# Optimization experiments

Measured on AMD Instinct MI355X. Metric: run time of the kernel, lower is better.

## Reference

```python
import jax, jax.numpy as jnp
import numpy as np

B, S, D, H, K = 1, 4096, 1024, 16, 64


def setup_inputs() -> dict:
    key = jax.random.key(0)
    ks = jax.random.split(key, 5)
    x = jax.random.normal(ks[0], (B, S, D), dtype=jnp.float32)
    wq = jax.random.normal(ks[1], (D, H, K), dtype=jnp.float32) / np.sqrt(D)
    wk = jax.random.normal(ks[2], (D, H, K), dtype=jnp.float32) / np.sqrt(D)
    wv = jax.random.normal(ks[3], (D, H, K), dtype=jnp.float32) / np.sqrt(D)
    wo = jax.random.normal(ks[4], (H, K, D), dtype=jnp.float32) / np.sqrt(H * K)
    bq = jnp.zeros((H, K), dtype=jnp.float32)
    bk = jnp.zeros((H, K), dtype=jnp.float32)
    bv = jnp.zeros((H, K), dtype=jnp.float32)
    bo = jnp.zeros((D,), dtype=jnp.float32)
    return {"x": x, "wq": wq, "bq": bq, "wk": wk, "bk": bk,
            "wv": wv, "bv": bv, "wo": wo, "bo": bo, "is_causal": 1}


def reference(x, wq, bq, wk, bk, wv, bv, wo, bo, is_causal):
    # QKV projections: [B,S,D] x [D,H,K] -> [B,S,H,K]
    q = jnp.einsum("bsd,dhk->bshk", x, wq) + bq
    k = jnp.einsum("bsd,dhk->bshk", x, wk) + bk
    v = jnp.einsum("bsd,dhk->bshk", x, wv) + bv
    # scores: [B,H,Q,KV], scaled by 1/sqrt(head_dim)
    scores = jnp.einsum("bqhk,bvhk->bhqv", q, k) / jnp.sqrt(jnp.float32(K))
    if is_causal:
        qpos = jnp.arange(S)[:, None]  # query position
        kpos = jnp.arange(S)[None, :]  # key position
        mask = (qpos >= kpos).astype(scores.dtype)  # [Q,KV]
        scores = scores - 1e9 * (1.0 - mask)
    probs = jax.nn.softmax(scores, axis=-1)
    # weighted values: [B,S,H,K]
    vals = jnp.einsum("bhqv,bvhk->bqhk", probs, v)
    # output projection: [B,S,H,K] x [H,K,D] -> [B,S,D]
    out = jnp.einsum("bqhk,hkd->bqd", vals, wo) + bo
    return out
```

## Files before the change

### kernel.cpp

```cpp
#include <hip/hip_runtime.h>

typedef _Float16 f16;
typedef f16 f16x8 __attribute__((ext_vector_type(8)));
typedef f16 f16x4 __attribute__((ext_vector_type(4)));
typedef float f32x2 __attribute__((ext_vector_type(2)));
typedef float f32x4 __attribute__((ext_vector_type(4)));
typedef float f32x16 __attribute__((ext_vector_type(16)));
typedef unsigned u32;

#define MFMA16(a, b, c) __builtin_amdgcn_mfma_f32_16x16x32_f16((a), (b), (c), 0, 0, 0)
#define MFMA32(a, b, c) __builtin_amdgcn_mfma_f32_32x32x16_f16((a), (b), (c), 0, 0, 0)

#define QSCL 0.18033688011f

#define WAITV(N) asm volatile("s_waitcnt vmcnt(" #N ")" ::: "memory")
#define BAR()                          \
  {                                    \
    __builtin_amdgcn_s_barrier();      \
    __builtin_amdgcn_sched_barrier(0); \
  }

__device__ __forceinline__ void gll16(const void* g, void* l) {
  __builtin_amdgcn_global_load_lds(
      (__attribute__((address_space(1))) unsigned int*)(void*)(g),
      (__attribute__((address_space(3))) unsigned int*)(l), 16, 0, 0);
}

__device__ __forceinline__ float ex2(float x) {
  float r;
  asm("v_exp_f32 %0, %1" : "=v"(r) : "v"(x));
  return r;
}

__device__ __forceinline__ void plswap(u32& a, u32& b) {
  asm("s_nop 1\n\tv_permlane32_swap_b32 %0, %1\n\ts_nop 1" : "+v"(a), "+v"(b));
}

__device__ __forceinline__ void plswap2(u32& a, u32& b, u32& c, u32& d) {
  asm("s_nop 1\n\tv_permlane32_swap_b32 %0, %1\n\tv_permlane32_swap_b32 %2, %3\n\ts_nop 1"
      : "+v"(a), "+v"(b), "+v"(c), "+v"(d));
}

__device__ __forceinline__ u32 pk16(float lo, float hi) {
  __fp16 h2[2];
  *(decltype(__builtin_amdgcn_cvt_pkrtz(0.f, 0.f))*)h2 =
      __builtin_amdgcn_cvt_pkrtz(lo, hi);
  return *(u32*)h2;
}

__global__ void k_prep(const float* __restrict__ x, f16* __restrict__ xb,
                       const float* __restrict__ wq, const float* __restrict__ wk,
                       const float* __restrict__ wv, const float* __restrict__ wo,
                       f16* __restrict__ wqkvT, f16* __restrict__ woT) {
  __shared__ float tile[64][65];
  const int bid = blockIdx.x;
  if (bid < 4096) {
    const int i = bid * 256 + threadIdx.x;
    float4 v = reinterpret_cast<const float4*>(x)[i];
    f16x4 o = {(f16)v.x, (f16)v.y, (f16)v.z, (f16)v.w};
    reinterpret_cast<f16x4*>(xb)[i] = o;
    return;
  }
  const int tb = bid - 4096;
  const int which = tb >> 8;
  const int bidx = tb & 255;
  const float* src = which == 0 ? wq : which == 1 ? wk : which == 2 ? wv : wo;
  f16* dst = which == 0 ? wqkvT
             : which == 1 ? wqkvT + (size_t)1024 * 1024
             : which == 2 ? wqkvT + (size_t)2048 * 1024
                          : woT;
  const int bc = bidx & 15, br = bidx >> 4;
  const int r0 = br << 6, c0 = bc << 6;
  const int tr = threadIdx.x >> 6, tc = threadIdx.x & 63;
#pragma unroll
  for (int p = 0; p < 16; ++p)
    tile[p * 4 + tr][tc] = src[(size_t)(r0 + p * 4 + tr) * 1024 + c0 + tc];
  __syncthreads();
#pragma unroll
  for (int p = 0; p < 16; ++p)
    dst[(size_t)(c0 + p * 4 + tr) * 1024 + r0 + tc] = (f16)tile[tc][p * 4 + tr];
}

template <int MODE, int NFR, int PAIR>
__global__ __launch_bounds__(256, 3) void k_gemm(
    const f16* __restrict__ A, const f16* __restrict__ Bt, int nbm, int Kd,
    const float* __restrict__ bias0, const float* __restrict__ bias1,
    const float* __restrict__ bias2,
    f16* __restrict__ Qo, f16* __restrict__ Ko, f16* __restrict__ Vo,
    float* __restrict__ Fo) {
  constexpr int TSZ = 8192 + NFR * 2048;
  constexpr int NBUF = PAIR ? 4 : 3;
  __shared__ __align__(16) char smem[NBUF * TSZ];
  const int tid = threadIdx.x;
  const int wid = tid >> 6, lane = tid & 63;
  const int r = lane & 15, t = lane >> 4;
  const int bm = blockIdx.x % nbm, bn = blockIdx.x / nbm;
  const int m0 = bm << 7, n0 = bn * (NFR * 32);
  const int wr = wid >> 1, wc = wid & 1;

  const f32x4 vz = {0.f, 0.f, 0.f, 0.f};
  f32x4 acc[4][NFR];
#pragma unroll
  for (int m = 0; m < 4; ++m)
#pragma unroll
    for (int n = 0; n < NFR; ++n) acc[m][n] = vz;

  const int srow = tid >> 2;
  const int scb = (((tid & 3) ^ ((tid >> 3) & 3)) << 4);
  const size_t ldb = (size_t)Kd * 2;
  const char* Ab = (const char*)A + (size_t)m0 * ldb + scb;
  const char* Bb = (const char*)Bt + (size_t)n0 * ldb + scb;

  auto issue = [&](int kt, int buf) {
    const size_t kb = (size_t)kt << 6;
    char* base = smem + buf * TSZ;
    gll16(Ab + (size_t)srow * ldb + kb, base + wid * 1024);
    gll16(Ab + (size_t)(srow + 64) * ldb + kb, base + 4096 + wid * 1024);
    gll16(Bb + (size_t)srow * ldb + kb, base + 8192 + wid * 1024);
    if (NFR == 4)
      gll16(Bb + (size_t)(srow + 64) * ldb + kb, base + 8192 + 4096 + wid * 1024);
  };

  const int swz = ((r >> 1) & 3) << 4;

  auto comp = [&](int buf) {
    const char* base = smem + buf * TSZ;
    f16x8 af[4], bg[NFR];
#pragma unroll
    for (int m = 0; m < 4; ++m)
      af[m] = *(const f16x8*)(base + ((wr * 64 + m * 16 + r) * 64 +
                                      ((t * 16) ^ swz)));
#pragma unroll
    for (int n = 0; n < NFR; ++n)
      bg[n] = *(const f16x8*)(base + 8192 +
                              ((wc * (NFR * 16) + n * 16 + r) * 64 +
                               ((t * 16) ^ swz)));
    __builtin_amdgcn_s_setprio(1);
#pragma unroll
    for (int m = 0; m < 4; ++m)
#pragma unroll
      for (int n = 0; n < NFR; ++n) acc[m][n] = MFMA16(af[m], bg[n], acc[m][n]);
    __builtin_amdgcn_s_setprio(0);
  };

  const int nk = Kd >> 5;
  if (PAIR) {
    issue(0, 0);
    issue(1, 1);
    const int nsup = nk >> 1;
    for (int T = 0; T < nsup; ++T) {
      WAITV(0);
      BAR();
      if (T + 1 < nsup) {
        issue(2 * T + 2, (2 * T + 2) & 3);
        issue(2 * T + 3, (2 * T + 3) & 3);
      }
      comp((2 * T) & 3);
      comp((2 * T + 1) & 3);
    }
  } else {
    issue(0, 0);
    issue(1, 1);
    int b = 0, bi = 2;
    for (int kt = 0; kt < nk; ++kt) {
      if (kt + 1 < nk) {
        if (NFR == 4) {
          WAITV(4);
        } else {
          WAITV(3);
        }
      } else {
        WAITV(0);
      }
      BAR();
      if (kt + 2 < nk) issue(kt + 2, bi);
      comp(b);
      b = (b == 2) ? 0 : b + 1;
      bi = (bi == 2) ? 0 : bi + 1;
    }
  }

#pragma unroll
  for (int m = 0; m < 4; ++m) {
    const int row0 = m0 + wr * 64 + m * 16 + t * 4;
#pragma unroll
    for (int n = 0; n < NFR; ++n) {
      const int gc = n0 + wc * (NFR * 16) + n * 16 + r;
      if (MODE == 0) {
        const float b2 = gc < 1024 ? bias0[gc]
                                   : (gc < 2048 ? bias1[gc - 1024] : bias2[gc - 2048]);
        float v[4];
#pragma unroll
        for (int i = 0; i < 4; ++i) v[i] = acc[m][n][i] + b2;
        if (gc < 1024) {
#pragma unroll
          for (int i = 0; i < 4; ++i)
            Qo[(size_t)(row0 + i) * 1024 + gc] = (f16)(v[i] * QSCL);
        } else if (gc < 2048) {
#pragma unroll
          for (int i = 0; i < 4; ++i)
            Ko[(size_t)(row0 + i) * 1024 + (gc - 1024)] = (f16)v[i];
        } else {
          f16x4 pk = {(f16)v[0], (f16)v[1], (f16)v[2], (f16)v[3]};
          *(f16x4*)(Vo + (size_t)(gc - 2048) * 4096 + row0) = pk;
        }
      } else {
        const float b2 = bias0[gc];
#pragma unroll
        for (int i = 0; i < 4; ++i)
          Fo[(size_t)(row0 + i) * 1024 + gc] = acc[m][n][i] + b2;
      }
    }
  }
}

__global__ __launch_bounds__(512, 4) void k_fattn(
    const f16* __restrict__ Q, const f16* __restrict__ Kb,
    const f16* __restrict__ Vt, f16* __restrict__ vals,
    const int* __restrict__ causp) {
  __shared__ uint4 ldsv[4128];
  char* lds = (char*)ldsv;
  const int tid = threadIdx.x;
  const int W = tid >> 6, lane = tid & 63;
  const int l31 = lane & 31, hi = lane >> 5;
  const int wq = W >> 1, wkv = W & 1;
  const int h = blockIdx.x & 15;
  const int idx = blockIdx.x >> 4;
  const int qt = idx < 16 ? 31 - idx : idx - 16;
  const int cz = *causp;
  const int Tmax = cz ? qt : 31;
  const int dw = wq - wkv;
  const int jmax_w = cz ? (2 * qt + (dw >= 2 ? 1 : 0) - (dw < 0 ? 1 : 0)) : 63;
  const bool maskd = cz && ((dw & 1) == 0);

  const size_t qrow = (size_t)((qt << 7) + (wq << 5) + l31) * 1024 + h * 64;
  f16x8 qf[4];
#pragma unroll
  for (int s = 0; s < 4; ++s) qf[s] = *(const f16x8*)(Q + qrow + 16 * s + 8 * hi);

  f32x16 o0, o1, zv;
#pragma unroll
  for (int e = 0; e < 16; ++e) { o0[e] = 0.f; o1[e] = 0.f; zv[e] = 0.f; }
  float Ls = 0.f;

  const int srw = lane >> 3, sch = lane & 7;
  const int ssw = (sch ^ srw) << 3;
  const char* kcur =
      (const char*)(Kb + (size_t)(8 * W + srw) * 1024 + h * 64 + ssw);
  const char* vcur =
      (const char*)(Vt + (size_t)(h * 64 + 8 * W + srw) * 4096 + ssw);

  auto issue = [&](int buf) {
    char* base = lds + buf * 16384 + W * 1024;
    gll16(kcur, base);
    gll16(vcur, base + 8192);
    kcur += (size_t)64 * 2048;
    vcur += 128;
  };

  const int krow = (wkv << 5) + l31, ksw = krow & 7;
  const int vsw = l31 & 7;
  int koff[4];
#pragma unroll
  for (int s = 0; s < 4; ++s)
    koff[s] = krow * 128 + (((2 * s + hi) ^ ksw) << 4);
  int voffA[2], voffB[2];
#pragma unroll
  for (int ks = 0; ks < 2; ++ks) {
    const int cl = 4 * wkv + 2 * ks + hi;
    voffA[ks] = l31 * 128 + ((cl ^ vsw) << 4);
    voffB[ks] = (32 + l31) * 128 + ((cl ^ vsw) << 4);
  }

  auto qk = [&](const char* Kbase) -> f32x16 {
    f16x8 af[4];
#pragma unroll
    for (int s = 0; s < 4; ++s)
      af[s] = *(const f16x8*)(Kbase + koff[s]);
    __builtin_amdgcn_s_setprio(1);
    f32x16 sc = MFMA32(af[0], qf[0], zv);
#pragma unroll
    for (int s = 1; s < 4; ++s) sc = MFMA32(af[s], qf[s], sc);
    __builtin_amdgcn_s_setprio(0);
    return sc;
  };

  auto fin = [&](int j, const char* Kbase, f32x16& sc) {
    const char* Vbase = Kbase + 8192;
    if (maskd && j == jmax_w) {
#pragma unroll
      for (int e = 0; e < 16; ++e) {
        const int kvr = (e & 3) + 8 * (e >> 2) + 4 * hi;
        if (kvr > l31) sc[e] = -1e9f;
      }
    }
    f32x2 p2[8];
#pragma unroll
    for (int e = 0; e < 8; ++e) {
      f32x2 t;
      t[0] = ex2(sc[2 * e]);
      t[1] = ex2(sc[2 * e + 1]);
      p2[e] = t;
    }
    {
      f32x2 a0 = p2[0] + p2[1];
      f32x2 a1 = p2[2] + p2[3];
      f32x2 a2 = p2[4] + p2[5];
      f32x2 a3 = p2[6] + p2[7];
      f32x2 b0 = a0 + a1;
      f32x2 b1 = a2 + a3;
      f32x2 c = b0 + b1;
      float s = c[0] + c[1];
      union { float f; u32 u; } ua, ub;
      ua.f = s; ub.f = s;
      plswap(ua.u, ub.u);
      Ls += ua.f + ub.f;
    }
#pragma unroll
    for (int ks = 0; ks < 2; ++ks) {
      u32 c0 = pk16(p2[4 * ks + 0][0], p2[4 * ks + 0][1]);
      u32 c1 = pk16(p2[4 * ks + 1][0], p2[4 * ks + 1][1]);
      u32 c2 = pk16(p2[4 * ks + 2][0], p2[4 * ks + 2][1]);
      u32 c3 = pk16(p2[4 * ks + 3][0], p2[4 * ks + 3][1]);
      plswap2(c0, c2, c1, c3);
      union { u32 w[4]; f16x8 v; } pa;
      pa.w[0] = c0; pa.w[1] = c1; pa.w[2] = c2; pa.w[3] = c3;
      const f16x8 vf0 = *(const f16x8*)(Vbase + voffA[ks]);
      const f16x8 vf1 = *(const f16x8*)(Vbase + voffB[ks]);
      __builtin_amdgcn_s_setprio(1);
      o0 = MFMA32(pa.v, vf0, o0);
      o1 = MFMA32(pa.v, vf1, o1);
      __builtin_amdgcn_s_setprio(0);
    }
  };

  issue(0);
  issue(1);

  for (int T = 0; T <= Tmax; ++T) {
    BAR();
    if (T < Tmax) {
      const int nb = 2 * ((T + 1) & 1);
      issue(nb);
      issue(nb + 1);
      WAITV(4);
    } else {
      WAITV(0);
    }
    const int cb = 2 * (T & 1);
    const char* bA = lds + cb * 16384;
    const char* bB = lds + (cb + 1) * 16384;
    const int jA = 2 * T, jB = 2 * T + 1;
    if (jB <= jmax_w) {
      f32x16 scA = qk(bA);
      f32x16 scB = qk(bB);
      fin(jA, bA, scA);
      fin(jB, bB, scB);
    } else if (jA <= jmax_w) {
      f32x16 scA = qk(bA);
      fin(jA, bA, scA);
    }
  }
  __syncthreads();

  float* obuf = (float*)lds;
  float* lsbuf = (float*)(lds + 32768);
  if (hi == 0) lsbuf[wq * 64 + wkv * 32 + l31] = Ls;
  if (wkv == 1) {
    float* base = obuf + wq * 2048;
#pragma unroll
    for (int dblk = 0; dblk < 2; ++dblk)
#pragma unroll
      for (int rg = 0; rg < 4; ++rg) {
        const f32x16& o = dblk ? o1 : o0;
        f32x4 t = {o[rg * 4 + 0], o[rg * 4 + 1], o[rg * 4 + 2], o[rg * 4 + 3]};
        *(f32x4*)(base + ((dblk * 4 + rg) * 64 + lane) * 4) = t;
      }
  }
  __syncthreads();
  if (wkv == 0) {
    float* base = obuf + wq * 2048;
#pragma unroll
    for (int dblk = 0; dblk < 2; ++dblk)
#pragma unroll
      for (int rg = 0; rg < 4; ++rg) {
        f32x4 t = *(f32x4*)(base + ((dblk * 4 + rg) * 64 + lane) * 4);
        f32x16& o = dblk ? o1 : o0;
#pragma unroll
        for (int i = 0; i < 4; ++i) o[rg * 4 + i] += t[i];
      }
    float inv[16];
#pragma unroll
    for (int e = 0; e < 16; ++e) {
      const int q = (e & 3) + 8 * (e >> 2) + 4 * hi;
      inv[e] = 1.0f / (lsbuf[wq * 64 + q] + lsbuf[wq * 64 + 32 + q]);
    }
    const int row0 = (qt << 7) + (wq << 5);
#pragma unroll
    for (int dblk = 0; dblk < 2; ++dblk) {
      const f32x16& o = dblk ? o1 : o0;
      const int col = h * 64 + 32 * dblk + l31;
#pragma unroll
      for (int e = 0; e < 16; ++e) {
        const int rr = row0 + (e & 3) + 8 * (e >> 2) + 4 * hi;
        vals[(size_t)rr * 1024 + col] = (f16)(o[e] * inv[e]);
      }
    }
  }
}

extern "C" void kernel_launch(void* const* d_in, const int* in_sizes, int n_in,
                              void* d_out, int out_size, void* d_ws, size_t ws_size,
                              hipStream_t stream) {
  const float* x = (const float*)d_in[0];
  const float* wq = (const float*)d_in[1];
  const float* bq = (const float*)d_in[2];
  const float* wk = (const float*)d_in[3];
  const float* bk = (const float*)d_in[4];
  const float* wv = (const float*)d_in[5];
  const float* bv = (const float*)d_in[6];
  const float* wo = (const float*)d_in[7];
  const float* bo = (const float*)d_in[8];
  const int* caus = (const int*)d_in[9];
  float* out = (float*)d_out;

  f16* xb = (f16*)d_ws;
  f16* wqkvT = xb + (size_t)4096 * 1024;
  f16* woT = wqkvT + (size_t)3072 * 1024;
  f16* Qb = woT + (size_t)1024 * 1024;
  f16* Kbuf = Qb + (size_t)4096 * 1024;
  f16* Vt = Kbuf + (size_t)4096 * 1024;
  f16* vals = Vt + (size_t)4096 * 1024;

  k_prep<<<5120, 256, 0, stream>>>(x, xb, wq, wk, wv, wo, wqkvT, woT);
  k_gemm<0, 4, 0><<<32 * 24, 256, 0, stream>>>(xb, wqkvT, 32, 1024, bq, bk, bv,
                                               Qb, Kbuf, Vt, nullptr);
  k_fattn<<<512, 512, 0, stream>>>(Qb, Kbuf, Vt, vals, caus);
  k_gemm<1, 2, 0><<<32 * 16, 256, 0, stream>>>(vals, woT, 32, 1024, bo, nullptr,
                                               nullptr, nullptr, nullptr,
                                               nullptr, out);
}
```

Before: 118.2 us.

## Use 256x256-tile 512-thread GEMM kernel for QKV projection

Adds a new QKV projection GEMM kernel that computes 256x256 output tiles with 8 waves per block, a triple-buffered LDS pipeline with swizzled layout, and direct global-to-LDS loads interleaved with MFMA issue. Larger tiles raise arithmetic intensity and cut redundant loads of A and B compared with the earlier 128x128 tile kernel. The grid drops to 192 blocks, fewer than the 256 CUs on the device, so some CUs sit idle and occupancy per CU falls to one large block with 96KB of LDS.

```diff
diff --git a/kernel.cpp b/kernel.cpp
--- a/kernel.cpp
+++ b/kernel.cpp
@@ -79,6 +79,127 @@
 #pragma unroll
   for (int p = 0; p < 16; ++p)
     dst[(size_t)(c0 + p * 4 + tr) * 1024 + r0 + tc] = (f16)tile[tc][p * 4 + tr];
+}
+
+__global__ __launch_bounds__(512) void k_gemm256(
+    const f16* __restrict__ A, const f16* __restrict__ Bt, int nbm, int Kd,
+    const float* __restrict__ bias0, const float* __restrict__ bias1,
+    const float* __restrict__ bias2, f16* __restrict__ Qo,
+    f16* __restrict__ Ko, f16* __restrict__ Vo) {
+  __shared__ __align__(16) char smem[98304];
+  const int tid = threadIdx.x;
+  const int w = tid >> 6, lane = tid & 63;
+  const int r = lane & 15, t = lane >> 4;
+  const int wr = w >> 2, wc = w & 3;
+  const int bm = blockIdx.x % nbm, bn = blockIdx.x / nbm;
+  const int m0 = bm << 8, n0 = bn << 8;
+
+  const f32x4 vz = {0.f, 0.f, 0.f, 0.f};
+  f32x4 acc[8][4];
+#pragma unroll
+  for (int m = 0; m < 8; ++m)
+#pragma unroll
+    for (int n = 0; n < 4; ++n) acc[m][n] = vz;
+
+  const int srow = tid >> 2, scc = tid & 3;
+  const int ssw = (scc ^ ((srow >> 1) & 3)) << 4;
+  const char* Asrc = (const char*)A + (size_t)(m0 + srow) * 2048 + ssw;
+  const char* Bsrc = (const char*)Bt + (size_t)(n0 + srow) * 2048 + ssw;
+
+  auto iss = [&](int q, int kt, char* buf) {
+    const size_t kb = (size_t)kt << 6;
+    if (q == 0)
+      gll16(Asrc + kb, buf + w * 1024);
+    else if (q == 1)
+      gll16(Asrc + (size_t)128 * 2048 + kb, buf + 8192 + w * 1024);
+    else if (q == 2)
+      gll16(Bsrc + kb, buf + 16384 + w * 1024);
+    else
+      gll16(Bsrc + (size_t)128 * 2048 + kb, buf + 24576 + w * 1024);
+  };
+
+  int aoff[8], boff[4];
+#pragma unroll
+  for (int m = 0; m < 8; ++m) {
+    const int rA = wr * 128 + m * 16 + r;
+    aoff[m] = (rA >> 7) * 8192 + (rA & 127) * 64 + ((t ^ ((rA >> 1) & 3)) << 4);
+  }
+#pragma unroll
+  for (int n = 0; n < 4; ++n) {
+    const int rB = wc * 64 + n * 16 + r;
+    boff[n] =
+        16384 + (rB >> 7) * 8192 + (rB & 127) * 64 + ((t ^ ((rB >> 1) & 3)) << 4);
+  }
+
+  const int NG = Kd >> 5;
+  iss(0, 0, smem);
+  iss(1, 0, smem);
+  iss(2, 0, smem);
+  iss(3, 0, smem);
+  {
+    char* b1 = smem + 32768;
+    iss(0, 1, b1);
+    iss(1, 1, b1);
+    iss(2, 1, b1);
+    iss(3, 1, b1);
+  }
+
+  for (int g = 0; g < NG; ++g) {
+    BAR();
+    if (g + 1 < NG) {
+      WAITV(4);
+    } else {
+      WAITV(0);
+    }
+    const char* base = smem + (g % 3) * 32768;
+    char* nbuf = smem + ((g + 2) % 3) * 32768;
+    const bool pf = (g + 2 < NG);
+    f16x8 bg[4];
+#pragma unroll
+    for (int q = 0; q < 4; ++q) {
+      if (q == 0) {
+#pragma unroll
+        for (int n = 0; n < 4; ++n) bg[n] = *(const f16x8*)(base + boff[n]);
+      }
+      f16x8 a0 = *(const f16x8*)(base + aoff[2 * q]);
+      f16x8 a1 = *(const f16x8*)(base + aoff[2 * q + 1]);
+      if (pf) iss(q, g + 2, nbuf);
+      BAR();
+      __builtin_amdgcn_s_setprio(1);
+#pragma unroll
+      for (int n = 0; n < 4; ++n) {
+        acc[2 * q][n] = MFMA16(a0, bg[n], acc[2 * q][n]);
+        acc[2 * q + 1][n] = MFMA16(a1, bg[n], acc[2 * q + 1][n]);
+      }
+      __builtin_amdgcn_s_setprio(0);
+    }
+  }
+
+#pragma unroll
+  for (int m = 0; m < 8; ++m) {
+    const int row0 = m0 + wr * 128 + m * 16 + t * 4;
+#pragma unroll
+    for (int n = 0; n < 4; ++n) {
+      const int gc = n0 + wc * 64 + n * 16 + r;
+      const float b2 = gc < 1024 ? bias0[gc]
+                                 : (gc < 2048 ? bias1[gc - 1024] : bias2[gc - 2048]);
+      float v[4];
+#pragma unroll
+      for (int i = 0; i < 4; ++i) v[i] = acc[m][n][i] + b2;
+      if (gc < 1024) {
+#pragma unroll
+        for (int i = 0; i < 4; ++i)
+          Qo[(size_t)(row0 + i) * 1024 + gc] = (f16)(v[i] * QSCL);
+      } else if (gc < 2048) {
+#pragma unroll
+        for (int i = 0; i < 4; ++i)
+          Ko[(size_t)(row0 + i) * 1024 + (gc - 1024)] = (f16)v[i];
+      } else {
+        f16x4 pk = {(f16)v[0], (f16)v[1], (f16)v[2], (f16)v[3]};
+        *(f16x4*)(Vo + (size_t)(gc - 2048) * 4096 + row0) = pk;
+      }
+    }
+  }
 }
 
 template <int MODE, int NFR, int PAIR>
@@ -433,8 +554,8 @@
   f16* vals = Vt + (size_t)4096 * 1024;
 
   k_prep<<<5120, 256, 0, stream>>>(x, xb, wq, wk, wv, wo, wqkvT, woT);
-  k_gemm<0, 4, 0><<<32 * 24, 256, 0, stream>>>(xb, wqkvT, 32, 1024, bq, bk, bv,
-                                               Qb, Kbuf, Vt, nullptr);
+  k_gemm256<<<16 * 12, 512, 0, stream>>>(xb, wqkvT, 16, 1024, bq, bk, bv, Qb,
+                                         Kbuf, Vt);
   k_fattn<<<512, 512, 0, stream>>>(Qb, Kbuf, Vt, vals, caus);
   k_gemm<1, 2, 0><<<32 * 16, 256, 0, stream>>>(vals, woT, 32, 1024, bo, nullptr,
                                                nullptr, nullptr, nullptr,
```

Result: slower. 122.3 us (+3.5%).
